# Kernel optimization log

Hardware: AMD Instinct MI355X
Metric: run time of the kernel (lower is better)

## Reference

```python
import jax, jax.numpy as jnp
import numpy as np

ALPHA = 1.0


def setup_inputs() -> dict:
    key = jax.random.key(0)
    k1, k2 = jax.random.split(key)
    N, K, D = 131072, 512, 512
    inputs = jax.random.normal(k1, (N, D), dtype=jnp.float32)
    # xavier-uniform style init for clusters
    limit = float(np.sqrt(6.0 / (K + D)))
    clusters = jax.random.uniform(k2, (K, D), dtype=jnp.float32, minval=-limit, maxval=limit)
    return {"inputs": inputs, "clusters": clusters}


def reference(inputs, clusters):
    # (same math as sum((x[:,None,:]-c)**2, -1), without the N x K x D intermediate)
    x2 = jnp.sum(inputs * inputs, axis=1, keepdims=True)          # [N, 1]
    c2 = jnp.sum(clusters * clusters, axis=1)[None, :]            # [1, K]
    d2 = jnp.maximum(x2 + c2 - 2.0 * (inputs @ clusters.T), 0.0)  # [N, K]
    q = 1.0 / (1.0 + d2 / ALPHA)
    q = q ** ((ALPHA + 1.0) / 2.0)
    return q / jnp.sum(q, axis=1, keepdims=True)
```

## Files before the change

kernel.cpp:

```cpp
#include <hip/hip_runtime.h>
#include <stdint.h>

#define NPTS 131072
#define DIM  512
#define KC   512
#define BM   128
#define BK   32
#define NKT  (DIM / BK)

typedef float f32x16 __attribute__((ext_vector_type(16)));
typedef float f32x4  __attribute__((ext_vector_type(4)));
typedef short bf16x8 __attribute__((ext_vector_type(8)));

__device__ __forceinline__ short f2bf(float f) {
  union { float f; unsigned u; } v; v.f = f;
  unsigned r = v.u + 0x7FFFu + ((v.u >> 16) & 1u);
  return (short)(r >> 16);
}

__device__ __forceinline__ bf16x8 pack8(f32x4 a, f32x4 b) {
  bf16x8 p;
  p[0] = f2bf(a.x); p[1] = f2bf(a.y); p[2] = f2bf(a.z); p[3] = f2bf(a.w);
  p[4] = f2bf(b.x); p[5] = f2bf(b.y); p[6] = f2bf(b.z); p[7] = f2bf(b.w);
  return p;
}

__device__ __forceinline__ float sq8(f32x4 a, f32x4 b) {
  return a.x*a.x + a.y*a.y + a.z*a.z + a.w*a.w
       + b.x*b.x + b.y*b.y + b.z*b.z + b.w*b.w;
}

__device__ __forceinline__ void gload_lds16(const short* g, short* l) {
  __builtin_amdgcn_global_load_lds(
      (const __attribute__((address_space(1))) unsigned int*)g,
      (__attribute__((address_space(3))) unsigned int*)l, 16, 0, 0);
}

__global__ void dec_pack(const float* __restrict__ C, short* __restrict__ Bp,
                         float* __restrict__ c2) {
  const int n    = blockIdx.x;
  const int lane = threadIdx.x;
  const float* src = C + (size_t)n * DIM + lane * 8;
  f32x4 v0 = *(const f32x4*)src;
  f32x4 v1 = *(const f32x4*)(src + 4);
  float s = sq8(v0, v1);
  #pragma unroll
  for (int m = 1; m < 64; m <<= 1) s += __shfl_xor(s, m, 64);
  if (lane == 0) c2[n] = s;
  const int kt = lane >> 2;
  const int sl = (lane & 3) ^ ((n >> 1) & 3);
  *(bf16x8*)(Bp + (size_t)kt * (KC * BK) + n * BK + sl * 8) = pack8(v0, v1);
}

__global__ __launch_bounds__(512, 2)
void dec_main(const float* __restrict__ X, const short* __restrict__ Bp,
              const float* __restrict__ c2g, float* __restrict__ out) {
  __shared__ short Abuf[2][BM * BK];
  __shared__ short Bbuf[2][KC * BK];
  __shared__ float x2arr[BM][4];
  __shared__ float x2tot[BM];
  __shared__ float rowpart[BM][4];
  __shared__ float rowinv[BM];

  const int tid  = threadIdx.x;
  const int lane = tid & 63;
  const int wave = tid >> 6;
  const int wm   = wave >> 2;
  const int wn   = wave & 3;
  const int h    = lane >> 5;
  const int l31  = lane & 31;
  const int row0 = blockIdx.x * BM;

  const int ar = tid >> 2;
  const int ac = tid & 3;
  const float* aptr = X + (size_t)(row0 + ar) * DIM + ac * 8;
  const int aoff = ar * BK + ((ac ^ ((ar >> 1) & 3)) << 3);

  f32x16 acc[2][4];
  #pragma unroll
  for (int i = 0; i < 2; ++i)
    #pragma unroll
    for (int j = 0; j < 4; ++j)
      acc[i][j] = (f32x16)0.f;

  float x2acc = 0.f;

  {
    #pragma unroll
    for (int i = 0; i < 4; ++i) {
      const int chunk = i * 8 + wave;
      gload_lds16(Bp + chunk * 512 + lane * 8, &Bbuf[0][chunk * 512 + lane * 8]);
    }
    f32x4 v0 = *(const f32x4*)aptr;
    f32x4 v1 = *(const f32x4*)(aptr + 4);
    x2acc += sq8(v0, v1);
    *(bf16x8*)&Abuf[0][aoff] = pack8(v0, v1);
  }
  __syncthreads();

  for (int kt = 0; kt < NKT; ++kt) {
    const int cur = kt & 1;
    f32x4 v0, v1;
    if (kt + 1 < NKT) {
      #pragma unroll
      for (int i = 0; i < 4; ++i) {
        const int chunk = i * 8 + wave;
        gload_lds16(Bp + (size_t)(kt + 1) * (KC * BK) + chunk * 512 + lane * 8,
                    &Bbuf[cur ^ 1][chunk * 512 + lane * 8]);
      }
      v0 = *(const f32x4*)(aptr + (kt + 1) * BK);
      v1 = *(const f32x4*)(aptr + (kt + 1) * BK + 4);
    }

    #pragma unroll
    for (int ks = 0; ks < 2; ++ks) {
      const int sl = ks * 2 + h;
      bf16x8 af[2], bfr[4];
      #pragma unroll
      for (int mt = 0; mt < 2; ++mt) {
        const int r = wm * 64 + mt * 32 + l31;
        af[mt] = *(const bf16x8*)&Abuf[cur][r * BK + ((sl ^ ((r >> 1) & 3)) << 3)];
      }
      #pragma unroll
      for (int nt = 0; nt < 4; ++nt) {
        const int n = wn * 128 + nt * 32 + l31;
        bfr[nt] = *(const bf16x8*)&Bbuf[cur][n * BK + ((sl ^ ((n >> 1) & 3)) << 3)];
      }
      #pragma unroll
      for (int mt = 0; mt < 2; ++mt)
        #pragma unroll
        for (int nt = 0; nt < 4; ++nt)
          acc[mt][nt] = __builtin_amdgcn_mfma_f32_32x32x16_bf16(
              af[mt], bfr[nt], acc[mt][nt], 0, 0, 0);
    }

    if (kt + 1 < NKT) {
      x2acc += sq8(v0, v1);
      *(bf16x8*)&Abuf[cur ^ 1][aoff] = pack8(v0, v1);
    }
    __syncthreads();
  }

  x2arr[ar][ac] = x2acc;
  __syncthreads();
  if (tid < BM)
    x2tot[tid] = x2arr[tid][0] + x2arr[tid][1] + x2arr[tid][2] + x2arr[tid][3];
  __syncthreads();

  float c2v[4];
  #pragma unroll
  for (int nt = 0; nt < 4; ++nt) c2v[nt] = c2g[wn * 128 + nt * 32 + l31];

  float rowq[2][16];
  #pragma unroll
  for (int mt = 0; mt < 2; ++mt) {
    #pragma unroll
    for (int r = 0; r < 16; ++r) {
      const int m = wm * 64 + mt * 32 + (r & 3) + 8 * (r >> 2) + 4 * h;
      const float x2m = x2tot[m];
      float s = 0.f;
      #pragma unroll
      for (int nt = 0; nt < 4; ++nt) {
        float d2 = x2m + c2v[nt] - 2.f * acc[mt][nt][r];
        d2 = fmaxf(d2, 0.f);
        float q = __builtin_amdgcn_rcpf(1.f + d2);
        acc[mt][nt][r] = q;
        s += q;
      }
      rowq[mt][r] = s;
    }
  }

  #pragma unroll
  for (int msk = 1; msk < 32; msk <<= 1) {
    #pragma unroll
    for (int mt = 0; mt < 2; ++mt)
      #pragma unroll
      for (int r = 0; r < 16; ++r)
        rowq[mt][r] += __shfl_xor(rowq[mt][r], msk, 64);
  }

  if (l31 == 0) {
    #pragma unroll
    for (int mt = 0; mt < 2; ++mt)
      #pragma unroll
      for (int r = 0; r < 16; ++r)
        rowpart[wm * 64 + mt * 32 + (r & 3) + 8 * (r >> 2) + 4 * h][wn] = rowq[mt][r];
  }
  __syncthreads();
  if (tid < BM)
    rowinv[tid] = __builtin_amdgcn_rcpf(rowpart[tid][0] + rowpart[tid][1] +
                                        rowpart[tid][2] + rowpart[tid][3]);
  __syncthreads();

  #pragma unroll
  for (int mt = 0; mt < 2; ++mt) {
    #pragma unroll
    for (int r = 0; r < 16; ++r) {
      const int m = wm * 64 + mt * 32 + (r & 3) + 8 * (r >> 2) + 4 * h;
      const float inv = rowinv[m];
      float* o = out + (size_t)(row0 + m) * KC + wn * 128 + l31;
      #pragma unroll
      for (int nt = 0; nt < 4; ++nt)
        o[nt * 32] = acc[mt][nt][r] * inv;
    }
  }
}

extern "C" void kernel_launch(void* const* d_in, const int* in_sizes, int n_in,
                              void* d_out, int out_size, void* d_ws, size_t ws_size,
                              hipStream_t stream) {
  const float* X = (const float*)d_in[0];
  const float* C = (const float*)d_in[1];
  float* out = (float*)d_out;

  short* Bp = (short*)d_ws;
  float* c2 = (float*)((char*)d_ws + (size_t)KC * DIM * 2);

  dec_pack<<<KC, 64, 0, stream>>>(C, Bp, c2);
  dec_main<<<NPTS / BM, 512, 0, stream>>>(X, Bp, c2, out);
}
```

Baseline: 184.8 us.

## Drop LDS staging and stream MFMA operands directly from global memory

Replaces the LDS double-buffered 128-row tile with 32-row blocks of 4 waves. Each wave loads its A and B fragments straight from global memory into registers, with B stored as plain row-major bf16. This removes LDS traffic and the per-k-step barriers, and the row-norm reduction now uses shuffles. In exchange, the B matrix is re-read from L2 by every block (four times as many blocks), and there is no software prefetch apart from loop unrolling.

```diff
diff --git a/kernel.cpp b/kernel.cpp
--- a/kernel.cpp
+++ b/kernel.cpp
@@ -4,9 +4,7 @@
 #define NPTS 131072
 #define DIM  512
 #define KC   512
-#define BM   128
-#define BK   32
-#define NKT  (DIM / BK)
+#define NKT  16
 
 typedef float f32x16 __attribute__((ext_vector_type(16)));
 typedef float f32x4  __attribute__((ext_vector_type(4)));
@@ -30,13 +28,7 @@
        + b.x*b.x + b.y*b.y + b.z*b.z + b.w*b.w;
 }
 
-__device__ __forceinline__ void gload_lds16(const short* g, short* l) {
-  __builtin_amdgcn_global_load_lds(
-      (const __attribute__((address_space(1))) unsigned int*)g,
-      (__attribute__((address_space(3))) unsigned int*)l, 16, 0, 0);
-}
-
-__global__ void dec_pack(const float* __restrict__ C, short* __restrict__ Bp,
+__global__ void dec_pack(const float* __restrict__ C, short* __restrict__ Bbf,
                          float* __restrict__ c2) {
   const int n    = blockIdx.x;
   const int lane = threadIdx.x;
@@ -47,163 +39,98 @@
   #pragma unroll
   for (int m = 1; m < 64; m <<= 1) s += __shfl_xor(s, m, 64);
   if (lane == 0) c2[n] = s;
-  const int kt = lane >> 2;
-  const int sl = (lane & 3) ^ ((n >> 1) & 3);
-  *(bf16x8*)(Bp + (size_t)kt * (KC * BK) + n * BK + sl * 8) = pack8(v0, v1);
+  *(bf16x8*)(Bbf + (size_t)n * DIM + lane * 8) = pack8(v0, v1);
 }
 
-__global__ __launch_bounds__(512, 2)
-void dec_main(const float* __restrict__ X, const short* __restrict__ Bp,
+__global__ __launch_bounds__(256, 3)
+void dec_main(const float* __restrict__ X, const short* __restrict__ Bbf,
               const float* __restrict__ c2g, float* __restrict__ out) {
-  __shared__ short Abuf[2][BM * BK];
-  __shared__ short Bbuf[2][KC * BK];
-  __shared__ float x2arr[BM][4];
-  __shared__ float x2tot[BM];
-  __shared__ float rowpart[BM][4];
-  __shared__ float rowinv[BM];
+  __shared__ float part[4][2][16];
 
   const int tid  = threadIdx.x;
   const int lane = tid & 63;
-  const int wave = tid >> 6;
-  const int wm   = wave >> 2;
-  const int wn   = wave & 3;
+  const int wn   = tid >> 6;
+  const int l31  = lane & 31;
   const int h    = lane >> 5;
-  const int l31  = lane & 31;
-  const int row0 = blockIdx.x * BM;
+  const int row0 = blockIdx.x * 32;
 
-  const int ar = tid >> 2;
-  const int ac = tid & 3;
-  const float* aptr = X + (size_t)(row0 + ar) * DIM + ac * 8;
-  const int aoff = ar * BK + ((ac ^ ((ar >> 1) & 3)) << 3);
+  const float* ap = X + (size_t)(row0 + l31) * DIM + h * 8;
+  const short* bp[4];
+  #pragma unroll
+  for (int nt = 0; nt < 4; ++nt)
+    bp[nt] = Bbf + (size_t)(wn * 128 + nt * 32 + l31) * DIM + h * 8;
 
-  f32x16 acc[2][4];
+  f32x16 acc[4];
   #pragma unroll
-  for (int i = 0; i < 2; ++i)
+  for (int nt = 0; nt < 4; ++nt) acc[nt] = (f32x16)0.f;
+
+  float x2 = 0.f;
+
+  #pragma unroll 4
+  for (int kt = 0; kt < NKT; ++kt) {
+    const int ko = kt * 32;
+    f32x4 a00 = *(const f32x4*)(ap + ko);
+    f32x4 a01 = *(const f32x4*)(ap + ko + 4);
+    f32x4 a10 = *(const f32x4*)(ap + ko + 16);
+    f32x4 a11 = *(const f32x4*)(ap + ko + 20);
+    bf16x8 b0[4], b1[4];
     #pragma unroll
-    for (int j = 0; j < 4; ++j)
-      acc[i][j] = (f32x16)0.f;
-
-  float x2acc = 0.f;
-
-  {
-    #pragma unroll
-    for (int i = 0; i < 4; ++i) {
-      const int chunk = i * 8 + wave;
-      gload_lds16(Bp + chunk * 512 + lane * 8, &Bbuf[0][chunk * 512 + lane * 8]);
-    }
-    f32x4 v0 = *(const f32x4*)aptr;
-    f32x4 v1 = *(const f32x4*)(aptr + 4);
-    x2acc += sq8(v0, v1);
-    *(bf16x8*)&Abuf[0][aoff] = pack8(v0, v1);
-  }
-  __syncthreads();
-
-  for (int kt = 0; kt < NKT; ++kt) {
-    const int cur = kt & 1;
-    f32x4 v0, v1;
-    if (kt + 1 < NKT) {
-      #pragma unroll
-      for (int i = 0; i < 4; ++i) {
-        const int chunk = i * 8 + wave;
-        gload_lds16(Bp + (size_t)(kt + 1) * (KC * BK) + chunk * 512 + lane * 8,
-                    &Bbuf[cur ^ 1][chunk * 512 + lane * 8]);
-      }
-      v0 = *(const f32x4*)(aptr + (kt + 1) * BK);
-      v1 = *(const f32x4*)(aptr + (kt + 1) * BK + 4);
+    for (int nt = 0; nt < 4; ++nt) {
+      b0[nt] = *(const bf16x8*)(bp[nt] + ko);
+      b1[nt] = *(const bf16x8*)(bp[nt] + ko + 16);
     }
 
+    bf16x8 af0 = pack8(a00, a01);
+    bf16x8 af1 = pack8(a10, a11);
+    x2 += sq8(a00, a01) + sq8(a10, a11);
+
     #pragma unroll
-    for (int ks = 0; ks < 2; ++ks) {
-      const int sl = ks * 2 + h;
-      bf16x8 af[2], bfr[4];
-      #pragma unroll
-      for (int mt = 0; mt < 2; ++mt) {
-        const int r = wm * 64 + mt * 32 + l31;
-        af[mt] = *(const bf16x8*)&Abuf[cur][r * BK + ((sl ^ ((r >> 1) & 3)) << 3)];
-      }
-      #pragma unroll
-      for (int nt = 0; nt < 4; ++nt) {
-        const int n = wn * 128 + nt * 32 + l31;
-        bfr[nt] = *(const bf16x8*)&Bbuf[cur][n * BK + ((sl ^ ((n >> 1) & 3)) << 3)];
-      }
-      #pragma unroll
-      for (int mt = 0; mt < 2; ++mt)
-        #pragma unroll
-        for (int nt = 0; nt < 4; ++nt)
-          acc[mt][nt] = __builtin_amdgcn_mfma_f32_32x32x16_bf16(
-              af[mt], bfr[nt], acc[mt][nt], 0, 0, 0);
-    }
-
-    if (kt + 1 < NKT) {
-      x2acc += sq8(v0, v1);
-      *(bf16x8*)&Abuf[cur ^ 1][aoff] = pack8(v0, v1);
-    }
-    __syncthreads();
+    for (int nt = 0; nt < 4; ++nt)
+      acc[nt] = __builtin_amdgcn_mfma_f32_32x32x16_bf16(af0, b0[nt], acc[nt], 0, 0, 0);
+    #pragma unroll
+    for (int nt = 0; nt < 4; ++nt)
+      acc[nt] = __builtin_amdgcn_mfma_f32_32x32x16_bf16(af1, b1[nt], acc[nt], 0, 0, 0);
   }
 
-  x2arr[ar][ac] = x2acc;
-  __syncthreads();
-  if (tid < BM)
-    x2tot[tid] = x2arr[tid][0] + x2arr[tid][1] + x2arr[tid][2] + x2arr[tid][3];
-  __syncthreads();
+  x2 += __shfl_xor(x2, 32, 64);
 
   float c2v[4];
   #pragma unroll
   for (int nt = 0; nt < 4; ++nt) c2v[nt] = c2g[wn * 128 + nt * 32 + l31];
 
-  float rowq[2][16];
+  float srow[16];
   #pragma unroll
-  for (int mt = 0; mt < 2; ++mt) {
+  for (int r = 0; r < 16; ++r) {
+    const int mbase = (r & 3) + 8 * (r >> 2);
+    const float x2m = __shfl(x2, mbase + 4 * h, 64);
+    float s = 0.f;
     #pragma unroll
-    for (int r = 0; r < 16; ++r) {
-      const int m = wm * 64 + mt * 32 + (r & 3) + 8 * (r >> 2) + 4 * h;
-      const float x2m = x2tot[m];
-      float s = 0.f;
-      #pragma unroll
-      for (int nt = 0; nt < 4; ++nt) {
-        float d2 = x2m + c2v[nt] - 2.f * acc[mt][nt][r];
-        d2 = fmaxf(d2, 0.f);
-        float q = __builtin_amdgcn_rcpf(1.f + d2);
-        acc[mt][nt][r] = q;
-        s += q;
-      }
-      rowq[mt][r] = s;
+    for (int nt = 0; nt < 4; ++nt) {
+      float d2 = fmaxf(x2m + c2v[nt] - 2.f * acc[nt][r], 0.f);
+      float q = __builtin_amdgcn_rcpf(1.f + d2);
+      acc[nt][r] = q;
+      s += q;
     }
-  }
-
-  #pragma unroll
-  for (int msk = 1; msk < 32; msk <<= 1) {
     #pragma unroll
-    for (int mt = 0; mt < 2; ++mt)
-      #pragma unroll
-      for (int r = 0; r < 16; ++r)
-        rowq[mt][r] += __shfl_xor(rowq[mt][r], msk, 64);
+    for (int msk = 1; msk < 32; msk <<= 1) s += __shfl_xor(s, msk, 64);
+    srow[r] = s;
   }
 
   if (l31 == 0) {
     #pragma unroll
-    for (int mt = 0; mt < 2; ++mt)
-      #pragma unroll
-      for (int r = 0; r < 16; ++r)
-        rowpart[wm * 64 + mt * 32 + (r & 3) + 8 * (r >> 2) + 4 * h][wn] = rowq[mt][r];
+    for (int r = 0; r < 16; ++r) part[wn][h][r] = srow[r];
   }
-  __syncthreads();
-  if (tid < BM)
-    rowinv[tid] = __builtin_amdgcn_rcpf(rowpart[tid][0] + rowpart[tid][1] +
-                                        rowpart[tid][2] + rowpart[tid][3]);
   __syncthreads();
 
   #pragma unroll
-  for (int mt = 0; mt < 2; ++mt) {
+  for (int r = 0; r < 16; ++r) {
+    const float tot = part[0][h][r] + part[1][h][r] + part[2][h][r] + part[3][h][r];
+    const float iv = __builtin_amdgcn_rcpf(tot);
+    const int m = (r & 3) + 8 * (r >> 2) + 4 * h;
+    float* o = out + (size_t)(row0 + m) * KC + wn * 128 + l31;
     #pragma unroll
-    for (int r = 0; r < 16; ++r) {
-      const int m = wm * 64 + mt * 32 + (r & 3) + 8 * (r >> 2) + 4 * h;
-      const float inv = rowinv[m];
-      float* o = out + (size_t)(row0 + m) * KC + wn * 128 + l31;
-      #pragma unroll
-      for (int nt = 0; nt < 4; ++nt)
-        o[nt * 32] = acc[mt][nt][r] * inv;
-    }
+    for (int nt = 0; nt < 4; ++nt)
+      o[nt * 32] = acc[nt][r] * iv;
   }
 }
 
@@ -214,9 +141,9 @@
   const float* C = (const float*)d_in[1];
   float* out = (float*)d_out;
 
-  short* Bp = (short*)d_ws;
-  float* c2 = (float*)((char*)d_ws + (size_t)KC * DIM * 2);
+  short* Bbf = (short*)d_ws;
+  float* c2  = (float*)((char*)d_ws + (size_t)KC * DIM * 2);
 
-  dec_pack<<<KC, 64, 0, stream>>>(C, Bp, c2);
-  dec_main<<<NPTS / BM, 512, 0, stream>>>(X, Bp, c2, out);
+  dec_pack<<<KC, 64, 0, stream>>>(C, Bbf, c2);
+  dec_main<<<NPTS / 32, 256, 0, stream>>>(X, Bbf, c2, out);
 }
```

New measurement: 410.0 us. 122% more time.
